# Kernel optimization log

Measured on AMD Instinct MI355X. Metric: run time of the kernel, lower is better.

## Reference

```python
import jax, jax.numpy as jnp
import numpy as np

TLEN, BSZ, HID = 64, 32, 1024
SLEN = 200
V_TGT = 32000
V_EXT = 2000
UNK = 0  # ext_dict UNK index, ignored in the onehot scatter


def setup_inputs() -> dict:
    key = jax.random.key(0)
    ks = jax.random.split(key, 6)
    hidden = jax.random.normal(ks[0], (TLEN, BSZ, HID), dtype=jnp.float32)
    attn = jax.random.uniform(ks[1], (TLEN, BSZ, SLEN), dtype=jnp.float32)
    attn = attn / jnp.sum(attn, axis=-1, keepdims=True)  # attention-like distribution
    copy_to_ext = jax.random.randint(ks[2], (SLEN, BSZ), 0, V_EXT)
    W_out = jax.random.normal(ks[3], (V_TGT, HID), dtype=jnp.float32) * 0.02
    b_out = jnp.zeros((V_TGT,), dtype=jnp.float32)
    w_copy = jax.random.normal(ks[4], (1, HID), dtype=jnp.float32) * 0.02
    b_copy = jnp.zeros((1,), dtype=jnp.float32)
    return {"hidden": hidden, "attn": attn, "copy_to_ext": copy_to_ext,
            "W_out": W_out, "b_out": b_out, "w_copy": w_copy, "b_copy": b_copy}


def _safe_log(v):
    return jnp.log(jnp.clip(v, 0.001, 1.0 - 0.001))


def reference(hidden, attn, copy_to_ext, W_out, b_out, w_copy, b_copy):
    tlen, bsz, hid = hidden.shape
    slen = attn.shape[-1]
    h = hidden.reshape(tlen * bsz, hid)
    a = attn.reshape(tlen * bsz, slen)

    # p(copy) gate
    copy = jax.nn.sigmoid(h @ w_copy.T + b_copy)            # [N, 1]
    # generator log-probs over tgt vocab
    logits = h @ W_out.T + b_out                            # [N, V_TGT]
    prob_log = jax.nn.log_softmax(logits, axis=-1)
    out_prob_log = prob_log + _safe_log(copy)

    # attention mass scaled by (1 - p(copy)) -- NOTE: matches source exactly
    mul_attn = a * (1.0 - copy)                             # [N, SLEN]
    mul_attn_b = mul_attn.reshape(tlen, bsz, slen).transpose(1, 0, 2)  # [B, T, S]
    idx = copy_to_ext.T                                     # [B, S]

    def per_batch(m, i):
        # m: [T, S], i: [S]; scatter-add attn mass into ext vocab, ignoring UNK
        valid = (i != UNK).astype(m.dtype)                  # onehot ignore_index
        return jax.ops.segment_sum((m * valid).T, i, num_segments=V_EXT).T  # [T, E]

    ext_copy_prob = jax.vmap(per_batch)(mul_attn_b, idx)    # [B, T, E]
    ext_copy_prob = ext_copy_prob.transpose(1, 0, 2).reshape(tlen * bsz, V_EXT)
    ext_copy_prob_log = _safe_log(ext_copy_prob)

    out = jnp.concatenate([out_prob_log, ext_copy_prob_log], axis=1)
    return out.reshape(tlen, bsz, V_TGT + V_EXT)
```

## Files before the change

kernel.cpp:

```cpp
#include <hip/hip_runtime.h>
#include <cstdint>
#include <cstddef>

#define TLEN 64
#define BSZ  32
#define NROW 2048
#define HID  1024
#define SLEN 200
#define VT   32000
#define VE   2000
#define OUTW 34000
#define NBN  250

typedef float  f32x4  __attribute__((ext_vector_type(4)));
typedef __bf16 bf16x4 __attribute__((ext_vector_type(4)));
typedef __bf16 bf16x8 __attribute__((ext_vector_type(8)));
typedef float  floatx4 __attribute__((ext_vector_type(4)));

__global__ void cvt_kernel(const float* __restrict__ src, __bf16* __restrict__ dst, int n4) {
  int i = blockIdx.x * blockDim.x + threadIdx.x;
  int stride = gridDim.x * blockDim.x;
  for (; i < n4; i += stride) {
    f32x4 v = ((const f32x4*)src)[i];
    bf16x4 o;
    o.x = (__bf16)v.x; o.y = (__bf16)v.y; o.z = (__bf16)v.z; o.w = (__bf16)v.w;
    ((bf16x4*)dst)[i] = o;
  }
}

__global__ __launch_bounds__(256) void gate_kernel(
    const float* __restrict__ h, const float* __restrict__ wc,
    const float* __restrict__ bc, __bf16* __restrict__ Hbf,
    float* __restrict__ logcopy, float* __restrict__ oneminus) {
  int row = blockIdx.x;
  int tid = threadIdx.x;
  f32x4 v  = ((const f32x4*)(h + (size_t)row * HID))[tid];
  f32x4 wv = ((const f32x4*)wc)[tid];
  bf16x4 o;
  o.x = (__bf16)v.x; o.y = (__bf16)v.y; o.z = (__bf16)v.z; o.w = (__bf16)v.w;
  ((bf16x4*)(Hbf + (size_t)row * HID))[tid] = o;
  float s = v.x * wv.x + v.y * wv.y + v.z * wv.z + v.w * wv.w;
  #pragma unroll
  for (int off = 32; off; off >>= 1) s += __shfl_down(s, off, 64);
  __shared__ float wsum[4];
  int lane = tid & 63, w = tid >> 6;
  if (lane == 0) wsum[w] = s;
  __syncthreads();
  if (tid == 0) {
    float x = wsum[0] + wsum[1] + wsum[2] + wsum[3] + bc[0];
    float pc = 1.f / (1.f + __expf(-x));
    float pcc = fminf(fmaxf(pc, 0.001f), 0.999f);
    logcopy[row]  = logf(pcc);
    oneminus[row] = 1.f - pc;
  }
}

#define BM 128
#define BN 128
#define BK 32

__device__ __forceinline__ void load_lds16(const __bf16* g, __bf16* s) {
  __builtin_amdgcn_global_load_lds(
      (const __attribute__((address_space(1))) void*)g,
      (__attribute__((address_space(3))) void*)s, 16, 0, 0);
}

__global__ __launch_bounds__(256) void gemm_kernel(
    const __bf16* __restrict__ A, const __bf16* __restrict__ B,
    const float* __restrict__ bias, float* __restrict__ out) {
  __shared__ __attribute__((aligned(16))) __bf16 As[BM * BK];
  __shared__ __attribute__((aligned(16))) __bf16 Bs[BN * BK];
  __shared__ float lM0[128], lS0[128], lM1[128], lS1[128];

  const int tid = threadIdx.x;
  const int bn = blockIdx.x;
  const int bm = blockIdx.y;
  const int K = HID;

  const __bf16* aptr0 = A + (size_t)(bm * BM + (tid >> 2)) * K + (tid & 3) * 8;
  const __bf16* aptr1 = aptr0 + (size_t)64 * K;
  const __bf16* bptr0 = B + (size_t)(bn * BN + (tid >> 2)) * K + (tid & 3) * 8;
  const __bf16* bptr1 = bptr0 + (size_t)64 * K;
  __bf16* alds0 = &As[tid * 8];
  __bf16* alds1 = &As[2048 + tid * 8];
  __bf16* blds0 = &Bs[tid * 8];
  __bf16* blds1 = &Bs[2048 + tid * 8];

  const int l  = tid & 63;
  const int w  = tid >> 6;
  const int wm = w & 1;
  const int wn = w >> 1;
  const int lr = l & 15;
  const int q  = l >> 4;

  const bf16x8* Asv = (const bf16x8*)As;
  const bf16x8* Bsv = (const bf16x8*)Bs;

  int aidx[4], bidx[4];
  #pragma unroll
  for (int i = 0; i < 4; i++) aidx[i] = (wm * 64 + i * 16 + lr) * 4 + q;
  #pragma unroll
  for (int j = 0; j < 4; j++) bidx[j] = (wn * 64 + j * 16 + lr) * 4 + q;

  floatx4 acc[4][4] = {};

  for (int kt = 0; kt < K; kt += BK) {
    load_lds16(aptr0 + kt, alds0);
    load_lds16(aptr1 + kt, alds1);
    load_lds16(bptr0 + kt, blds0);
    load_lds16(bptr1 + kt, blds1);
    __syncthreads();

    bf16x8 af[4], bfr[4];
    #pragma unroll
    for (int i = 0; i < 4; i++) af[i] = Asv[aidx[i]];
    #pragma unroll
    for (int j = 0; j < 4; j++) bfr[j] = Bsv[bidx[j]];

    #pragma unroll
    for (int i = 0; i < 4; i++)
      #pragma unroll
      for (int j = 0; j < 4; j++)
        acc[i][j] = __builtin_amdgcn_mfma_f32_16x16x32_bf16(af[i], bfr[j], acc[i][j], 0, 0, 0);

    __syncthreads();
  }

  const int col0 = bn * BN + wn * 64 + lr;
  const int row0 = bm * BM + wm * 64 + q * 4;
  float bv[4];
  #pragma unroll
  for (int j = 0; j < 4; j++) bv[j] = bias[col0 + j * 16];

  #pragma unroll
  for (int i = 0; i < 4; i++) {
    #pragma unroll
    for (int r = 0; r < 4; r++) {
      int m = row0 + i * 16 + r;
      float* po = out + (size_t)m * OUTW + col0;
      float vj[4];
      #pragma unroll
      for (int j = 0; j < 4; j++) vj[j] = acc[i][j][r] + bv[j];
      #pragma unroll
      for (int j = 0; j < 4; j++) po[j * 16] = vj[j];
      float m4 = fmaxf(fmaxf(vj[0], vj[1]), fmaxf(vj[2], vj[3]));
      #pragma unroll
      for (int off = 1; off < 16; off <<= 1) m4 = fmaxf(m4, __shfl_xor(m4, off, 64));
      float s4 = __expf(vj[0] - m4) + __expf(vj[1] - m4) +
                 __expf(vj[2] - m4) + __expf(vj[3] - m4);
      #pragma unroll
      for (int off = 1; off < 16; off <<= 1) s4 += __shfl_xor(s4, off, 64);
      if (lr == 0) {
        int rl = wm * 64 + i * 16 + q * 4 + r;
        if (wn == 0) { lM0[rl] = m4; lS0[rl] = s4; }
        else         { lM1[rl] = m4; lS1[rl] = s4; }
      }
    }
  }
  __syncthreads();
  if (w == 0) {
    for (int e = l; e < 128; e += 64) {
      float Ma = lM0[e], Sa = lS0[e], Mb = lM1[e], Sb = lS1[e];
      float nm = fmaxf(Ma, Mb);
      float Sc = Sa * __expf(Ma - nm) + Sb * __expf(Mb - nm);
      int m = bm * BM + e;
      float2* pp = (float2*)(out + (size_t)m * OUTW + VT);
      pp[bn] = make_float2(nm, Sc);
    }
  }
}

__global__ __launch_bounds__(256) void finish_kernel(
    const float* __restrict__ attn, const int* __restrict__ c2e,
    const float* __restrict__ logcopy, const float* __restrict__ oneminus,
    float* __restrict__ out) {
  __shared__ float ext[VE];
  __shared__ float rM[4], rS[4];
  int row = blockIdx.x;
  int tid = threadIdx.x;
  int b = row & (BSZ - 1);
  float* orow = out + (size_t)row * OUTW;

  for (int e = tid; e < VE; e += 256) ext[e] = 0.f;

  float M = -3.0e38f, S = 0.f;
  if (tid < NBN) {
    float2 p = ((const float2*)(orow + VT))[tid];
    M = p.x; S = p.y;
  }
  #pragma unroll
  for (int off = 32; off; off >>= 1) {
    float om = __shfl_down(M, off, 64);
    float os = __shfl_down(S, off, 64);
    float nm = fmaxf(M, om);
    S = S * __expf(M - nm) + os * __expf(om - nm);
    M = nm;
  }
  int lane = tid & 63, w = tid >> 6;
  if (lane == 0) { rM[w] = M; rS[w] = S; }
  __syncthreads();
  float Mf = rM[0], Sf = rS[0];
  #pragma unroll
  for (int i = 1; i < 4; i++) {
    float nm = fmaxf(Mf, rM[i]);
    Sf = Sf * __expf(Mf - nm) + rS[i] * __expf(rM[i] - nm);
    Mf = nm;
  }
  float sub = Mf + logf(Sf) - logcopy[row];

  float om1 = oneminus[row];
  if (tid < SLEN) {
    int idx = c2e[tid * BSZ + b];
    if (idx != 0)
      atomicAdd(&ext[idx], attn[(size_t)row * SLEN + tid] * om1);
  }

  #pragma unroll 4
  for (int k2 = 0; k2 < 31; k2++) {
    f32x4* p = (f32x4*)orow + (tid + k2 * 256);
    f32x4 v = *p;
    v = v - sub;
    *p = v;
  }
  orow[31744 + tid] -= sub;

  __syncthreads();
  for (int e = tid; e < VE; e += 256)
    orow[VT + e] = logf(fminf(fmaxf(ext[e], 0.001f), 0.999f));
}

extern "C" void kernel_launch(void* const* d_in, const int* in_sizes, int n_in,
                              void* d_out, int out_size, void* d_ws, size_t ws_size,
                              hipStream_t stream) {
  const float* hidden = (const float*)d_in[0];
  const float* attn   = (const float*)d_in[1];
  const int*   c2e    = (const int*)d_in[2];
  const float* W      = (const float*)d_in[3];
  const float* bout   = (const float*)d_in[4];
  const float* wc     = (const float*)d_in[5];
  const float* bc     = (const float*)d_in[6];
  float* out = (float*)d_out;

  char* ws = (char*)d_ws;
  __bf16* Hbf = (__bf16*)ws;
  __bf16* Wbf = (__bf16*)(ws + 4194304);
  float* logcopy  = (float*)(ws + 4194304 + 65536000);
  float* oneminus = logcopy + NROW;

  cvt_kernel<<<4096, 256, 0, stream>>>(W, Wbf, (VT * HID) / 4);
  gate_kernel<<<NROW, 256, 0, stream>>>(hidden, wc, bc, Hbf, logcopy, oneminus);
  gemm_kernel<<<dim3(VT / BN, NROW / BM), 256, 0, stream>>>(Hbf, Wbf, bout, out);
  finish_kernel<<<NROW, 256, 0, stream>>>(attn, c2e, logcopy, oneminus, out);
}
```

Measured before the change: 696.9 us.

## Fuse prep kernels, drop softmax max tracking, use nontemporal memory ops

Merges the weight conversion and gate kernels into one launch with block-range dispatch. Removes the running max from the partial softmax, summing raw exponentials, which removes shuffles and exps but risks overflow for large logits. Adds nontemporal loads and stores on the large output write and rewrite passes to reduce cache pollution.

```diff
diff --git a/kernel.cpp b/kernel.cpp
--- a/kernel.cpp
+++ b/kernel.cpp
@@ -17,41 +17,42 @@
 typedef __bf16 bf16x8 __attribute__((ext_vector_type(8)));
 typedef float  floatx4 __attribute__((ext_vector_type(4)));
 
-__global__ void cvt_kernel(const float* __restrict__ src, __bf16* __restrict__ dst, int n4) {
-  int i = blockIdx.x * blockDim.x + threadIdx.x;
-  int stride = gridDim.x * blockDim.x;
-  for (; i < n4; i += stride) {
-    f32x4 v = ((const f32x4*)src)[i];
+__global__ __launch_bounds__(256) void prep_kernel(
+    const float* __restrict__ h, const float* __restrict__ wc,
+    const float* __restrict__ bc, const float* __restrict__ W,
+    __bf16* __restrict__ Hbf, __bf16* __restrict__ Wbf,
+    float* __restrict__ logcopy, float* __restrict__ oneminus) {
+  int tid = threadIdx.x;
+  if (blockIdx.x < NROW) {
+    int row = blockIdx.x;
+    f32x4 v  = ((const f32x4*)(h + (size_t)row * HID))[tid];
+    f32x4 wv = ((const f32x4*)wc)[tid];
     bf16x4 o;
     o.x = (__bf16)v.x; o.y = (__bf16)v.y; o.z = (__bf16)v.z; o.w = (__bf16)v.w;
-    ((bf16x4*)dst)[i] = o;
-  }
-}
-
-__global__ __launch_bounds__(256) void gate_kernel(
-    const float* __restrict__ h, const float* __restrict__ wc,
-    const float* __restrict__ bc, __bf16* __restrict__ Hbf,
-    float* __restrict__ logcopy, float* __restrict__ oneminus) {
-  int row = blockIdx.x;
-  int tid = threadIdx.x;
-  f32x4 v  = ((const f32x4*)(h + (size_t)row * HID))[tid];
-  f32x4 wv = ((const f32x4*)wc)[tid];
-  bf16x4 o;
-  o.x = (__bf16)v.x; o.y = (__bf16)v.y; o.z = (__bf16)v.z; o.w = (__bf16)v.w;
-  ((bf16x4*)(Hbf + (size_t)row * HID))[tid] = o;
-  float s = v.x * wv.x + v.y * wv.y + v.z * wv.z + v.w * wv.w;
-  #pragma unroll
-  for (int off = 32; off; off >>= 1) s += __shfl_down(s, off, 64);
-  __shared__ float wsum[4];
-  int lane = tid & 63, w = tid >> 6;
-  if (lane == 0) wsum[w] = s;
-  __syncthreads();
-  if (tid == 0) {
-    float x = wsum[0] + wsum[1] + wsum[2] + wsum[3] + bc[0];
-    float pc = 1.f / (1.f + __expf(-x));
-    float pcc = fminf(fmaxf(pc, 0.001f), 0.999f);
-    logcopy[row]  = logf(pcc);
-    oneminus[row] = 1.f - pc;
+    ((bf16x4*)(Hbf + (size_t)row * HID))[tid] = o;
+    float s = v.x * wv.x + v.y * wv.y + v.z * wv.z + v.w * wv.w;
+    #pragma unroll
+    for (int off = 32; off; off >>= 1) s += __shfl_down(s, off, 64);
+    __shared__ float wsum[4];
+    int lane = tid & 63, w = tid >> 6;
+    if (lane == 0) wsum[w] = s;
+    __syncthreads();
+    if (tid == 0) {
+      float x = wsum[0] + wsum[1] + wsum[2] + wsum[3] + bc[0];
+      float pc = 1.f / (1.f + __expf(-x));
+      float pcc = fminf(fmaxf(pc, 0.001f), 0.999f);
+      logcopy[row]  = logf(pcc);
+      oneminus[row] = 1.f - pc;
+    }
+  } else {
+    const int n4 = (VT * HID) / 4;
+    int i = (blockIdx.x - NROW) * 256 + tid;
+    for (; i < n4; i += 4096 * 256) {
+      f32x4 v = __builtin_nontemporal_load(((const f32x4*)W) + i);
+      bf16x4 o;
+      o.x = (__bf16)v.x; o.y = (__bf16)v.y; o.z = (__bf16)v.z; o.w = (__bf16)v.w;
+      ((bf16x4*)Wbf)[i] = o;
+    }
   }
 }
 
@@ -70,7 +71,7 @@
     const float* __restrict__ bias, float* __restrict__ out) {
   __shared__ __attribute__((aligned(16))) __bf16 As[BM * BK];
   __shared__ __attribute__((aligned(16))) __bf16 Bs[BN * BK];
-  __shared__ float lM0[128], lS0[128], lM1[128], lS1[128];
+  __shared__ float lS0[128], lS1[128];
 
   const int tid = threadIdx.x;
   const int bn = blockIdx.x;
@@ -142,30 +143,24 @@
       #pragma unroll
       for (int j = 0; j < 4; j++) vj[j] = acc[i][j][r] + bv[j];
       #pragma unroll
-      for (int j = 0; j < 4; j++) po[j * 16] = vj[j];
-      float m4 = fmaxf(fmaxf(vj[0], vj[1]), fmaxf(vj[2], vj[3]));
-      #pragma unroll
-      for (int off = 1; off < 16; off <<= 1) m4 = fmaxf(m4, __shfl_xor(m4, off, 64));
-      float s4 = __expf(vj[0] - m4) + __expf(vj[1] - m4) +
-                 __expf(vj[2] - m4) + __expf(vj[3] - m4);
+      for (int j = 0; j < 4; j++) __builtin_nontemporal_store(vj[j], po + j * 16);
+      float s4 = __expf(vj[0]) + __expf(vj[1]) + __expf(vj[2]) + __expf(vj[3]);
       #pragma unroll
       for (int off = 1; off < 16; off <<= 1) s4 += __shfl_xor(s4, off, 64);
       if (lr == 0) {
         int rl = wm * 64 + i * 16 + q * 4 + r;
-        if (wn == 0) { lM0[rl] = m4; lS0[rl] = s4; }
-        else         { lM1[rl] = m4; lS1[rl] = s4; }
+        if (wn == 0) lS0[rl] = s4; else lS1[rl] = s4;
       }
     }
   }
   __syncthreads();
   if (w == 0) {
-    for (int e = l; e < 128; e += 64) {
-      float Ma = lM0[e], Sa = lS0[e], Mb = lM1[e], Sb = lS1[e];
-      float nm = fmaxf(Ma, Mb);
-      float Sc = Sa * __expf(Ma - nm) + Sb * __expf(Mb - nm);
+    #pragma unroll
+    for (int e0 = 0; e0 < 128; e0 += 64) {
+      int e = e0 + l;
+      float S = lS0[e] + lS1[e];
       int m = bm * BM + e;
-      float2* pp = (float2*)(out + (size_t)m * OUTW + VT);
-      pp[bn] = make_float2(nm, Sc);
+      __builtin_nontemporal_store(S, out + (size_t)m * OUTW + VT + bn);
     }
   }
 }
@@ -175,7 +170,7 @@
     const float* __restrict__ logcopy, const float* __restrict__ oneminus,
     float* __restrict__ out) {
   __shared__ float ext[VE];
-  __shared__ float rM[4], rS[4];
+  __shared__ float rS[4];
   int row = blockIdx.x;
   int tid = threadIdx.x;
   int b = row & (BSZ - 1);
@@ -183,30 +178,13 @@
 
   for (int e = tid; e < VE; e += 256) ext[e] = 0.f;
 
-  float M = -3.0e38f, S = 0.f;
-  if (tid < NBN) {
-    float2 p = ((const float2*)(orow + VT))[tid];
-    M = p.x; S = p.y;
-  }
-  #pragma unroll
-  for (int off = 32; off; off >>= 1) {
-    float om = __shfl_down(M, off, 64);
-    float os = __shfl_down(S, off, 64);
-    float nm = fmaxf(M, om);
-    S = S * __expf(M - nm) + os * __expf(om - nm);
-    M = nm;
-  }
+  float S = (tid < NBN) ? orow[VT + tid] : 0.f;
+  #pragma unroll
+  for (int off = 32; off; off >>= 1) S += __shfl_down(S, off, 64);
   int lane = tid & 63, w = tid >> 6;
-  if (lane == 0) { rM[w] = M; rS[w] = S; }
+  if (lane == 0) rS[w] = S;
   __syncthreads();
-  float Mf = rM[0], Sf = rS[0];
-  #pragma unroll
-  for (int i = 1; i < 4; i++) {
-    float nm = fmaxf(Mf, rM[i]);
-    Sf = Sf * __expf(Mf - nm) + rS[i] * __expf(rM[i] - nm);
-    Mf = nm;
-  }
-  float sub = Mf + logf(Sf) - logcopy[row];
+  float sub = logf(rS[0] + rS[1] + rS[2] + rS[3]) - logcopy[row];
 
   float om1 = oneminus[row];
   if (tid < SLEN) {
@@ -218,15 +196,19 @@
   #pragma unroll 4
   for (int k2 = 0; k2 < 31; k2++) {
     f32x4* p = (f32x4*)orow + (tid + k2 * 256);
-    f32x4 v = *p;
+    f32x4 v = __builtin_nontemporal_load(p);
     v = v - sub;
-    *p = v;
-  }
-  orow[31744 + tid] -= sub;
+    __builtin_nontemporal_store(v, p);
+  }
+  {
+    float v = __builtin_nontemporal_load(orow + 31744 + tid);
+    __builtin_nontemporal_store(v - sub, orow + 31744 + tid);
+  }
 
   __syncthreads();
   for (int e = tid; e < VE; e += 256)
-    orow[VT + e] = logf(fminf(fmaxf(ext[e], 0.001f), 0.999f));
+    __builtin_nontemporal_store(logf(fminf(fmaxf(ext[e], 0.001f), 0.999f)),
+                                orow + VT + e);
 }
 
 extern "C" void kernel_launch(void* const* d_in, const int* in_sizes, int n_in,
@@ -247,8 +229,8 @@
   float* logcopy  = (float*)(ws + 4194304 + 65536000);
   float* oneminus = logcopy + NROW;
 
-  cvt_kernel<<<4096, 256, 0, stream>>>(W, Wbf, (VT * HID) / 4);
-  gate_kernel<<<NROW, 256, 0, stream>>>(hidden, wc, bc, Hbf, logcopy, oneminus);
+  prep_kernel<<<NROW + 4096, 256, 0, stream>>>(hidden, wc, bc, W, Hbf, Wbf,
+                                               logcopy, oneminus);
   gemm_kernel<<<dim3(VT / BN, NROW / BM), 256, 0, stream>>>(Hbf, Wbf, bout, out);
   finish_kernel<<<NROW, 256, 0, stream>>>(attn, c2e, logcopy, oneminus, out);
 }
```

Result: no change. 686.3 us (-1.5%).
